# Performance work log

Hardware: AMD Instinct MI355X
Metric: run time of the kernel (lower is better)

Reference implementation:

```python
import jax, jax.numpy as jnp
import numpy as np

HEAD_SIZE = 64
INPUT_SIZE = 1024
B, T = 4, 4096


def setup_inputs() -> dict:
    key = jax.random.key(0)
    ks = jax.random.split(key, 7)
    s = 1.0 / np.sqrt(INPUT_SIZE)
    return {
        "x": jax.random.normal(ks[0], (B, T, INPUT_SIZE), dtype=jnp.float32),
        "Wk": jax.random.uniform(ks[1], (INPUT_SIZE, HEAD_SIZE), jnp.float32, -s, s),
        "bk": jax.random.uniform(ks[2], (HEAD_SIZE,), jnp.float32, -s, s),
        "Wq": jax.random.uniform(ks[3], (INPUT_SIZE, HEAD_SIZE), jnp.float32, -s, s),
        "bq": jax.random.uniform(ks[4], (HEAD_SIZE,), jnp.float32, -s, s),
        "Wv": jax.random.uniform(ks[5], (INPUT_SIZE, HEAD_SIZE), jnp.float32, -s, s),
        "bv": jax.random.uniform(ks[6], (HEAD_SIZE,), jnp.float32, -s, s),
    }


def reference(x, Wk, bk, Wq, bq, Wv, bv) -> jnp.ndarray:
    # x: [B, T, D]
    Tlen = x.shape[1]
    k = x @ Wk + bk          # [B, T, H]
    q = x @ Wq + bq          # [B, T, H]
    v = x @ Wv + bv          # [B, T, H]
    scale = 1.0 / jnp.sqrt(jnp.float32(HEAD_SIZE))
    # NOTE: original computes k @ q^T (not q @ k^T) -- keep that exact math.
    w = jnp.einsum("bth,bsh->bts", k, q) * scale  # [B, T, T]
    causal = jnp.tril(jnp.ones((Tlen, Tlen), dtype=bool))
    w = jnp.where(causal, w, -jnp.inf)
    w = jax.nn.softmax(w, axis=-1)
    out = jnp.einsum("bts,bsh->bth", w, v)        # [B, T, H]
    return out
```

## Files before the change

kernel.cpp:

```cpp
#include <hip/hip_runtime.h>
#include <hip/hip_bf16.h>
#include <stdint.h>

typedef __attribute__((ext_vector_type(8))) short short8;
typedef __attribute__((ext_vector_type(4))) float floatx4;

#define HD 64
#define D_IN 1024
#define TLEN 4096
#define NB 4
#define PPB 144
#define LDP 72
#define SL2E 0.18033688011112042f

__device__ __forceinline__ short f2bf(float f) {
    union { float f; uint32_t u; } v{f};
    uint32_t u = v.u;
    uint32_t r = (u + 0x7FFFu + ((u >> 16) & 1u)) >> 16;
    return (short)r;
}

__device__ __forceinline__ uint32_t pk2(float a, float b) {
    __hip_bfloat162 h = __float22bfloat162_rn(float2{a, b});
    union { __hip_bfloat162 h; uint32_t u; } c{h};
    return c.u;
}

__device__ __forceinline__ void ld_lds16(const void* g, void* l) {
    __builtin_amdgcn_global_load_lds(
        (const __attribute__((address_space(1))) uint32_t*)g,
        (__attribute__((address_space(3))) uint32_t*)l, 16, 0, 0);
}

__global__ __launch_bounds__(256) void prep_w(const float* __restrict__ Wk,
                                              const float* __restrict__ Wq,
                                              const float* __restrict__ Wv,
                                              short* __restrict__ wt) {
    int i = blockIdx.x * 256 + threadIdx.x;
    int j  = i & 7;
    int l  = (i >> 3) & 63;
    int ks = (i >> 9) & 1;
    int rest = i >> 10;
    int f  = rest % 12;
    int kt = rest / 12;
    int mat = f >> 2, nt = f & 3;
    int n = nt * 16 + (l & 15);
    int k = kt * 64 + ks * 32 + (l >> 4) * 8 + j;
    const float* W = (mat == 0) ? Wk : ((mat == 1) ? Wq : Wv);
    wt[i] = f2bf(W[(size_t)k * 64 + n]);
}

__global__ __launch_bounds__(256) void proj(const float* __restrict__ x,
                                            const float* __restrict__ bk,
                                            const float* __restrict__ bq,
                                            const float* __restrict__ bv,
                                            const short* __restrict__ wt,
                                            short* __restrict__ ko,
                                            short* __restrict__ qo,
                                            short* __restrict__ vt) {
    __shared__ float xs[2][2048];
    __shared__ short ws2[2][12288];

    int tid = threadIdx.x;
    int wave = tid >> 6, lane = tid & 63;
    int quad = lane >> 4, l16 = lane & 15;
    int row0 = blockIdx.x * 32;
    int wbase = tid & ~63;

    floatx4 acc[2][3];
#pragma unroll
    for (int mt = 0; mt < 2; mt++)
#pragma unroll
        for (int fi = 0; fi < 3; fi++) acc[mt][fi] = (floatx4){0.f, 0.f, 0.f, 0.f};

    auto stage = [&](int kt, int buf) {
#pragma unroll
        for (int it = 0; it < 2; it++) {
            int s = it * 256 + tid;
            int r = s >> 4, p = s & 15;
            int c = (((p >> 1) ^ (r & 7)) << 1) | (p & 1);
            ld_lds16(x + (size_t)(row0 + r) * D_IN + kt * 64 + c * 4,
                     &xs[buf][(it * 256 + wbase) * 4]);
        }
#pragma unroll
        for (int it = 0; it < 6; it++) {
            int s = it * 256 + tid;
            ld_lds16(wt + (size_t)kt * 12288 + (size_t)s * 8,
                     &ws2[buf][(it * 256 + wbase) * 8]);
        }
    };

    stage(0, 0);
    for (int kt = 0; kt < 16; kt++) {
        int buf = kt & 1;
        __syncthreads();
        if (kt < 15) stage(kt + 1, buf ^ 1);
#pragma unroll
        for (int ks = 0; ks < 2; ks++) {
            short8 av[2];
#pragma unroll
            for (int mt = 0; mt < 2; mt++) {
                int r = mt * 16 + l16;
                int g = ks * 4 + quad;
                const float4* pp = reinterpret_cast<const float4*>(
                    &xs[buf][r * 64 + ((g ^ (r & 7)) << 1) * 4]);
                float4 f0 = pp[0], f1 = pp[1];
                union { uint32_t u[4]; short8 s; } cv;
                cv.u[0] = pk2(f0.x, f0.y); cv.u[1] = pk2(f0.z, f0.w);
                cv.u[2] = pk2(f1.x, f1.y); cv.u[3] = pk2(f1.z, f1.w);
                av[mt] = cv.s;
            }
#pragma unroll
            for (int fi = 0; fi < 3; fi++) {
                int f = wave * 3 + fi;
                short8 bf = *reinterpret_cast<const short8*>(
                    &ws2[buf][((f * 2 + ks) * 64 + lane) * 8]);
#pragma unroll
                for (int mt = 0; mt < 2; mt++)
                    acc[mt][fi] = __builtin_amdgcn_mfma_f32_16x16x32_bf16(av[mt], bf, acc[mt][fi], 0, 0, 0);
            }
        }
    }

#pragma unroll
    for (int fi = 0; fi < 3; fi++) {
        int f = wave * 3 + fi;
        int mat = f >> 2, nt = f & 3;
        int col = nt * 16 + l16;
        const float* bias = (mat == 0) ? bk : ((mat == 1) ? bq : bv);
        float bb = bias[col];
#pragma unroll
        for (int mt = 0; mt < 2; mt++)
#pragma unroll
            for (int reg = 0; reg < 4; reg++) {
                float v = acc[mt][fi][reg] + bb;
                int row = row0 + mt * 16 + quad * 4 + reg;
                if (mat == 0) ko[(size_t)row * HD + col] = f2bf(v * SL2E);
                else if (mat == 1) qo[(size_t)row * HD + col] = f2bf(v);
                else {
                    int bt = row >> 12, tl = row & 4095;
                    vt[(size_t)bt * HD * TLEN + (size_t)col * TLEN + tl] = f2bf(v);
                }
            }
    }
}

template<int SPLIT>
__global__ __launch_bounds__(256) void attn_kern(const short* __restrict__ kb,
                                                 const short* __restrict__ qb,
                                                 const short* __restrict__ vtw,
                                                 float* __restrict__ dst,
                                                 float* __restrict__ pL) {
    __shared__ short Ks[2][4096];
    __shared__ short Vs[2][4096];
    __shared__ short Ps[128 * LDP];

    int tid = threadIdx.x;
    int wave = tid >> 6, lane = tid & 63;
    int quad = lane >> 4, l16 = lane & 15;
    int wbase = tid & ~63;
    int batch = blockIdx.y;

    int tile, j0, j1, slot = 0;
    if (SPLIT) {
        int bx = blockIdx.x;
        int t = 0, accb = 0;
        for (;;) { int p = (2 * t + 9) >> 3; if (bx < accb + p) break; accb += p; ++t; }
        tile = t;
        j0 = (bx - accb) * 8;
        int je = j0 + 8, lim = 2 * tile + 2;
        j1 = je < lim ? je : lim;
        slot = batch * PPB + bx;
    } else {
        tile = 31 - blockIdx.x;
        j0 = 0; j1 = 2 * tile + 2;
    }
    int t0 = tile * 128;
    int jd = 2 * tile;
    size_t base = (size_t)batch * TLEN * HD;
    const short* vbase = vtw + (size_t)batch * HD * TLEN;

    short8 kf[2][2];
#pragma unroll
    for (int mt = 0; mt < 2; mt++) {
        int trow = t0 + wave * 32 + mt * 16 + l16;
#pragma unroll
        for (int ks = 0; ks < 2; ks++)
            kf[mt][ks] = *reinterpret_cast<const short8*>(kb + base + (size_t)trow * HD + ks * 32 + quad * 8);
    }

    floatx4 o_acc[2][4];
#pragma unroll
    for (int mt = 0; mt < 2; mt++)
#pragma unroll
        for (int ht = 0; ht < 4; ht++) o_acc[mt][ht] = (floatx4){0.f, 0.f, 0.f, 0.f};
    float l_p[2] = {0.f, 0.f};

    auto stage = [&](int j, int buf) {
        int s0 = j * 64;
#pragma unroll
        for (int it = 0; it < 2; it++) {
            int s = it * 256 + tid;
            int r = s >> 3, c = (s & 7) ^ (r & 7);
            ld_lds16(qb + base + (size_t)(s0 + r) * HD + c * 8,
                     &Ks[buf][(it * 256 + wbase) * 8]);
            ld_lds16(vbase + (size_t)r * TLEN + s0 + c * 8,
                     &Vs[buf][(it * 256 + wbase) * 8]);
        }
    };

    stage(j0, 0);
    for (int j = j0; j < j1; ++j) {
        int buf = (j - j0) & 1;
        __syncthreads();
        if (j + 1 < j1) stage(j + 1, buf ^ 1);

        floatx4 sacc[2][4];
#pragma unroll
        for (int mt = 0; mt < 2; mt++)
#pragma unroll
            for (int nt = 0; nt < 4; nt++) sacc[mt][nt] = (floatx4){0.f, 0.f, 0.f, 0.f};
#pragma unroll
        for (int ks = 0; ks < 2; ks++)
#pragma unroll
            for (int nt = 0; nt < 4; nt++) {
                int r = nt * 16 + l16, g = ks * 4 + quad;
                short8 a = *reinterpret_cast<const short8*>(
                    &Ks[buf][r * 64 + (g ^ (r & 7)) * 8]);
#pragma unroll
                for (int mt = 0; mt < 2; mt++)
                    sacc[mt][nt] = __builtin_amdgcn_mfma_f32_16x16x32_bf16(a, kf[mt][ks], sacc[mt][nt], 0, 0, 0);
            }

        float pv[2][4][4];
#pragma unroll
        for (int mt = 0; mt < 2; mt++)
#pragma unroll
            for (int nt = 0; nt < 4; nt++)
#pragma unroll
                for (int reg = 0; reg < 4; reg++)
                    pv[mt][nt][reg] = __builtin_amdgcn_exp2f(sacc[mt][nt][reg]);
        if (j >= jd) {
            int s0 = j * 64;
#pragma unroll
            for (int mt = 0; mt < 2; mt++) {
                int t_g = t0 + wave * 32 + mt * 16 + l16;
#pragma unroll
                for (int nt = 0; nt < 4; nt++) {
                    int s_g = s0 + nt * 16 + quad * 4;
#pragma unroll
                    for (int reg = 0; reg < 4; reg++)
                        if (s_g + reg > t_g) pv[mt][nt][reg] = 0.f;
                }
            }
        }
#pragma unroll
        for (int mt = 0; mt < 2; mt++) {
            l_p[mt] += ((pv[mt][0][0] + pv[mt][0][1]) + (pv[mt][0][2] + pv[mt][0][3]))
                     + ((pv[mt][1][0] + pv[mt][1][1]) + (pv[mt][1][2] + pv[mt][1][3]))
                     + ((pv[mt][2][0] + pv[mt][2][1]) + (pv[mt][2][2] + pv[mt][2][3]))
                     + ((pv[mt][3][0] + pv[mt][3][1]) + (pv[mt][3][2] + pv[mt][3][3]));
#pragma unroll
            for (int nt = 0; nt < 4; nt++) {
                union { uint32_t u[2]; uint64_t q; } w;
                w.u[0] = pk2(pv[mt][nt][0], pv[mt][nt][1]);
                w.u[1] = pk2(pv[mt][nt][2], pv[mt][nt][3]);
                int row = wave * 32 + mt * 16 + l16;
                *reinterpret_cast<uint64_t*>(&Ps[row * LDP + nt * 16 + quad * 4]) = w.q;
            }
        }

#pragma unroll
        for (int ks = 0; ks < 2; ks++) {
            short8 a[2];
#pragma unroll
            for (int mt = 0; mt < 2; mt++)
                a[mt] = *reinterpret_cast<const short8*>(
                    &Ps[(wave * 32 + mt * 16 + l16) * LDP + ks * 32 + quad * 8]);
#pragma unroll
            for (int ht = 0; ht < 4; ht++) {
                int r = ht * 16 + l16, g = ks * 4 + quad;
                short8 b = *reinterpret_cast<const short8*>(
                    &Vs[buf][r * 64 + (g ^ (r & 7)) * 8]);
#pragma unroll
                for (int mt = 0; mt < 2; mt++)
                    o_acc[mt][ht] = __builtin_amdgcn_mfma_f32_16x16x32_bf16(a[mt], b, o_acc[mt][ht], 0, 0, 0);
            }
        }
    }

#pragma unroll
    for (int mt = 0; mt < 2; mt++) {
        l_p[mt] += __shfl_xor(l_p[mt], 16);
        l_p[mt] += __shfl_xor(l_p[mt], 32);
    }

    if (SPLIT) {
        float* po = dst + (size_t)slot * 8192;
#pragma unroll
        for (int mt = 0; mt < 2; mt++)
#pragma unroll
            for (int ht = 0; ht < 4; ht++)
#pragma unroll
                for (int reg = 0; reg < 4; reg++) {
                    int lr = wave * 32 + mt * 16 + quad * 4 + reg;
                    po[lr * 64 + ht * 16 + l16] = o_acc[mt][ht][reg];
                }
        if (quad == 0) {
#pragma unroll
            for (int mt = 0; mt < 2; mt++)
                pL[(size_t)slot * 128 + wave * 32 + mt * 16 + l16] = l_p[mt];
        }
    } else {
#pragma unroll
        for (int mt = 0; mt < 2; mt++) {
#pragma unroll
            for (int reg = 0; reg < 4; reg++) {
                float L = __shfl(l_p[mt], quad * 4 + reg, 64);
                float inv = 1.0f / L;
                int t = t0 + wave * 32 + mt * 16 + quad * 4 + reg;
#pragma unroll
                for (int ht = 0; ht < 4; ht++)
                    dst[base + (size_t)t * HD + ht * 16 + l16] = o_acc[mt][ht][reg] * inv;
            }
        }
    }
}

__global__ __launch_bounds__(256) void attn_combine(const float* __restrict__ pO,
                                                    const float* __restrict__ pL,
                                                    float* __restrict__ out) {
    int tile = blockIdx.x, batch = blockIdx.y;
    int nparts = (2 * tile + 9) >> 3;
    int a = tile >> 2, r = tile & 3;
    int slot0 = batch * PPB + 2 * a * (a + 1) + r * (a + 1);
    int t = threadIdx.x;
    int off = t * 32;
    int row = off >> 6;

    float L = 0.f;
    float4 acc[8];
#pragma unroll
    for (int i = 0; i < 8; i++) acc[i] = (float4){0.f, 0.f, 0.f, 0.f};

    for (int p = 0; p < nparts; ++p) {
        int slot = slot0 + p;
        L += pL[(size_t)slot * 128 + row];
        const float4* src = reinterpret_cast<const float4*>(pO + (size_t)slot * 8192 + off);
#pragma unroll
        for (int i = 0; i < 8; i++) {
            float4 v = src[i];
            acc[i].x += v.x; acc[i].y += v.y; acc[i].z += v.z; acc[i].w += v.w;
        }
    }
    float inv = 1.0f / L;
    float4* dstp = reinterpret_cast<float4*>(out + (size_t)batch * TLEN * HD +
                                             (size_t)tile * 128 * HD + off);
#pragma unroll
    for (int i = 0; i < 8; i++) {
        float4 v; v.x = acc[i].x * inv; v.y = acc[i].y * inv; v.z = acc[i].z * inv; v.w = acc[i].w * inv;
        dstp[i] = v;
    }
}

extern "C" void kernel_launch(void* const* d_in, const int* in_sizes, int n_in,
                              void* d_out, int out_size, void* d_ws, size_t ws_size,
                              hipStream_t stream) {
    const float* x  = (const float*)d_in[0];
    const float* Wk = (const float*)d_in[1];
    const float* bk = (const float*)d_in[2];
    const float* Wq = (const float*)d_in[3];
    const float* bq = (const float*)d_in[4];
    const float* Wv = (const float*)d_in[5];
    const float* bv = (const float*)d_in[6];
    float* out = (float*)d_out;

    const size_t nrow = (size_t)NB * TLEN;
    short* ko = (short*)d_ws;
    short* qo = ko + nrow * HD;
    short* vt = qo + nrow * HD;
    short* wt = vt + nrow * HD;
    float* pO = (float*)(wt + 3 * 64 * 1024);
    float* pL = pO + (size_t)NB * PPB * 8192;
    size_t need = (size_t)((char*)(pL + (size_t)NB * PPB * 128) - (char*)d_ws);

    prep_w<<<768, 256, 0, stream>>>(Wk, Wq, Wv, wt);
    proj<<<512, 256, 0, stream>>>(x, bk, bq, bv, wt, ko, qo, vt);
    if (ws_size >= need) {
        attn_kern<1><<<dim3(PPB, NB), 256, 0, stream>>>(ko, qo, vt, pO, pL);
        attn_combine<<<dim3(32, NB), 256, 0, stream>>>(pO, pL, out);
    } else {
        attn_kern<0><<<dim3(32, NB), 256, 0, stream>>>(ko, qo, vt, out, nullptr);
    }
}
```

Before: 156.4 us.

## Fuse split-K combine into attention kernel via last-block atomic counter

Removes the separate attn_combine launch. Each split block now publishes its partial output and row sums, issues a threadfence, and bumps a per-tile atomic counter that prep_w zeroes; the last-arriving block for a tile reduces all partials and writes the normalized output. Separately, waves 0 and 1 skip the final key chunk of the diagonal tile, since every key in it is causally masked for their query rows. This saves a launch and a kernel boundary, at the cost of fences, an atomic, and a serialized reduction tail in one block per tile; the wave-divergent skip could conflict with any barriers inside the loop body.

```diff
diff --git a/kernel.cpp b/kernel.cpp
--- a/kernel.cpp
+++ b/kernel.cpp
@@ -35,7 +35,9 @@
 __global__ __launch_bounds__(256) void prep_w(const float* __restrict__ Wk,
                                               const float* __restrict__ Wq,
                                               const float* __restrict__ Wv,
-                                              short* __restrict__ wt) {
+                                              short* __restrict__ wt,
+                                              int* __restrict__ pCnt) {
+    if (blockIdx.x == 0 && threadIdx.x < NB * 32) pCnt[threadIdx.x] = 0;
     int i = blockIdx.x * 256 + threadIdx.x;
     int j  = i & 7;
     int l  = (i >> 3) & 63;
@@ -150,10 +152,13 @@
                                                  const short* __restrict__ qb,
                                                  const short* __restrict__ vtw,
                                                  float* __restrict__ dst,
-                                                 float* __restrict__ pL) {
+                                                 float* __restrict__ pL,
+                                                 int* __restrict__ pCnt,
+                                                 float* __restrict__ out) {
     __shared__ short Ks[2][4096];
     __shared__ short Vs[2][4096];
     __shared__ short Ps[128 * LDP];
+    __shared__ int s_flag;
 
     int tid = threadIdx.x;
     int wave = tid >> 6, lane = tid & 63;
@@ -161,7 +166,7 @@
     int wbase = tid & ~63;
     int batch = blockIdx.y;
 
-    int tile, j0, j1, slot = 0;
+    int tile, j0, j1, slot = 0, slot0 = 0, nparts = 0;
     if (SPLIT) {
         int bx = blockIdx.x;
         int t = 0, accb = 0;
@@ -171,6 +176,8 @@
         int je = j0 + 8, lim = 2 * tile + 2;
         j1 = je < lim ? je : lim;
         slot = batch * PPB + bx;
+        slot0 = batch * PPB + accb;
+        nparts = (2 * tile + 9) >> 3;
     } else {
         tile = 31 - blockIdx.x;
         j0 = 0; j1 = 2 * tile + 2;
@@ -215,6 +222,8 @@
         __syncthreads();
         if (j + 1 < j1) stage(j + 1, buf ^ 1);
 
+        if (j == jd + 1 && wave < 2) continue;
+
         floatx4 sacc[2][4];
 #pragma unroll
         for (int mt = 0; mt < 2; mt++)
@@ -311,6 +320,37 @@
             for (int mt = 0; mt < 2; mt++)
                 pL[(size_t)slot * 128 + wave * 32 + mt * 16 + l16] = l_p[mt];
         }
+        __threadfence();
+        __syncthreads();
+        if (tid == 0) s_flag = atomicAdd(&pCnt[batch * 32 + tile], 1);
+        __syncthreads();
+        if (s_flag == nparts - 1) {
+            __threadfence();
+            int off = tid * 32;
+            int row = off >> 6;
+            float L = 0.f;
+            float4 acc2[8];
+#pragma unroll
+            for (int i = 0; i < 8; i++) acc2[i] = (float4){0.f, 0.f, 0.f, 0.f};
+            for (int p = 0; p < nparts; ++p) {
+                int sl = slot0 + p;
+                L += pL[(size_t)sl * 128 + row];
+                const float4* src = reinterpret_cast<const float4*>(dst + (size_t)sl * 8192 + off);
+#pragma unroll
+                for (int i = 0; i < 8; i++) {
+                    float4 v = src[i];
+                    acc2[i].x += v.x; acc2[i].y += v.y; acc2[i].z += v.z; acc2[i].w += v.w;
+                }
+            }
+            float inv = 1.0f / L;
+            float4* dstp = reinterpret_cast<float4*>(out + base + (size_t)t0 * HD + off);
+#pragma unroll
+            for (int i = 0; i < 8; i++) {
+                float4 v; v.x = acc2[i].x * inv; v.y = acc2[i].y * inv;
+                v.z = acc2[i].z * inv; v.w = acc2[i].w * inv;
+                dstp[i] = v;
+            }
+        }
     } else {
 #pragma unroll
         for (int mt = 0; mt < 2; mt++) {
@@ -324,42 +364,6 @@
                     dst[base + (size_t)t * HD + ht * 16 + l16] = o_acc[mt][ht][reg] * inv;
             }
         }
-    }
-}
-
-__global__ __launch_bounds__(256) void attn_combine(const float* __restrict__ pO,
-                                                    const float* __restrict__ pL,
-                                                    float* __restrict__ out) {
-    int tile = blockIdx.x, batch = blockIdx.y;
-    int nparts = (2 * tile + 9) >> 3;
-    int a = tile >> 2, r = tile & 3;
-    int slot0 = batch * PPB + 2 * a * (a + 1) + r * (a + 1);
-    int t = threadIdx.x;
-    int off = t * 32;
-    int row = off >> 6;
-
-    float L = 0.f;
-    float4 acc[8];
-#pragma unroll
-    for (int i = 0; i < 8; i++) acc[i] = (float4){0.f, 0.f, 0.f, 0.f};
-
-    for (int p = 0; p < nparts; ++p) {
-        int slot = slot0 + p;
-        L += pL[(size_t)slot * 128 + row];
-        const float4* src = reinterpret_cast<const float4*>(pO + (size_t)slot * 8192 + off);
-#pragma unroll
-        for (int i = 0; i < 8; i++) {
-            float4 v = src[i];
-            acc[i].x += v.x; acc[i].y += v.y; acc[i].z += v.z; acc[i].w += v.w;
-        }
-    }
-    float inv = 1.0f / L;
-    float4* dstp = reinterpret_cast<float4*>(out + (size_t)batch * TLEN * HD +
-                                             (size_t)tile * 128 * HD + off);
-#pragma unroll
-    for (int i = 0; i < 8; i++) {
-        float4 v; v.x = acc[i].x * inv; v.y = acc[i].y * inv; v.z = acc[i].z * inv; v.w = acc[i].w * inv;
-        dstp[i] = v;
     }
 }
 
@@ -382,14 +386,14 @@
     short* wt = vt + nrow * HD;
     float* pO = (float*)(wt + 3 * 64 * 1024);
     float* pL = pO + (size_t)NB * PPB * 8192;
-    size_t need = (size_t)((char*)(pL + (size_t)NB * PPB * 128) - (char*)d_ws);
-
-    prep_w<<<768, 256, 0, stream>>>(Wk, Wq, Wv, wt);
+    int*  pCnt = (int*)(pL + (size_t)NB * PPB * 128);
+    size_t need = (size_t)((char*)(pCnt + NB * 32) - (char*)d_ws);
+
+    prep_w<<<768, 256, 0, stream>>>(Wk, Wq, Wv, wt, pCnt);
     proj<<<512, 256, 0, stream>>>(x, bk, bq, bv, wt, ko, qo, vt);
     if (ws_size >= need) {
-        attn_kern<1><<<dim3(PPB, NB), 256, 0, stream>>>(ko, qo, vt, pO, pL);
-        attn_combine<<<dim3(32, NB), 256, 0, stream>>>(pO, pL, out);
+        attn_kern<1><<<dim3(PPB, NB), 256, 0, stream>>>(ko, qo, vt, pO, pL, pCnt, out);
     } else {
-        attn_kern<0><<<dim3(32, NB), 256, 0, stream>>>(ko, qo, vt, out, nullptr);
-    }
-}
+        attn_kern<0><<<dim3(32, NB), 256, 0, stream>>>(ko, qo, vt, out, nullptr, nullptr, out);
+    }
+}
```

Result: slower. 257.1 us (+64.4%).
